# Kernel optimization log

Hardware: AMD Instinct MI355X
Metric: run time of the kernel (lower is better)

The kernel has to match this reference:

```python
import jax, jax.numpy as jnp
import numpy as np

B, T, HS, H, R = 4, 2048, 1024, 16, 16
D = HS // H  # 64 head_dim
LOGIT_01 = float(np.log(0.1 / 0.9))    # g_proj bias init
LOGIT_098 = float(np.log(0.98 / 0.02)) # base decay logits init


def _rope_cos_sin(seq_len, dim, base=10000.0):
    half = dim // 2
    inv_freq = 1.0 / (base ** (jnp.arange(half, dtype=jnp.float32) / half))
    freqs = jnp.arange(seq_len, dtype=jnp.float32)[:, None] * inv_freq[None, :]  # [T, half]
    return jnp.cos(freqs), jnp.sin(freqs)


def _apply_rope(x, cos, sin):
    # x: [B,T,H,D] with D even; rotate interleaved pairs over full D
    c = cos[None, :, None, :]
    s = sin[None, :, None, :]
    x1 = x[..., 0::2]
    x2 = x[..., 1::2]
    r1 = x1 * c - x2 * s
    r2 = x1 * s + x2 * c
    return jnp.stack((r1, r2), axis=-1).reshape(x.shape)


def setup_inputs() -> dict:
    key = jax.random.key(0)
    ks = jax.random.split(key, 10)
    def rn(k, shape, s=0.02):
        return jax.random.normal(k, shape, dtype=jnp.float32) * s
    return {
        "x": jax.random.normal(ks[0], (B, T, HS), dtype=jnp.float32),
        "q_w": rn(ks[1], (HS, HS)),
        "k_w": rn(ks[2], (HS, HS)),
        "v_w": rn(ks[3], (HS, HS)),
        "Wq": rn(ks[4], (H, R, D), 0.05),
        "Wk": rn(ks[5], (H, R, D), 0.05),
        "g_w": rn(ks[6], (H * R, HS)),
        "g_b": jnp.full((H * R,), LOGIT_01, dtype=jnp.float32),
        "base_decay_logits": jnp.full((H, R), LOGIT_098, dtype=jnp.float32),
        "out_w": rn(ks[7], (HS, HS)),
        "out_b": jnp.zeros((HS,), dtype=jnp.float32),
        "ln_g": jnp.ones((HS,), dtype=jnp.float32),
        "ln_b": jnp.zeros((HS,), dtype=jnp.float32),
    }


def reference(x, q_w, k_w, v_w, Wq, Wk, g_w, g_b, base_decay_logits,
              out_w, out_b, ln_g, ln_b):
    b, t, hs = x.shape
    h, r, d = Wq.shape
    # qkv projections (torch Linear: x @ W.T)
    q = (x @ q_w.T).reshape(b, t, h, d)
    k = (x @ k_w.T).reshape(b, t, h, d)
    v = (x @ v_w.T).reshape(b, t, h, d)
    # RoPE (dim_rot == head_dim since it is even)
    cos, sin = _rope_cos_sin(t, d)
    q = _apply_rope(q, cos, sin)
    k = _apply_rope(k, cos, sin)
    # low-rank projections
    q_r = jnp.einsum('bthd,hrd->bthr', q, Wq)
    k_r = jnp.einsum('bthd,hrd->bthr', k, Wk)
    # content gates
    g = jax.nn.sigmoid((x @ g_w.T + g_b).reshape(b, t, h, r))
    decay = jax.nn.sigmoid(base_decay_logits)[None, :, :, None]  # [1,H,r,1]
    scale = 1.0 / jnp.sqrt(jnp.asarray(d, dtype=x.dtype))

    def step(M, inp):
        q_t, k_t, v_t, g_t = inp  # [B,H,r], [B,H,r], [B,H,D], [B,H,r]
        M = M * decay + jnp.einsum('bhr,bhd->bhrd', g_t * k_t * scale, v_t)
        y = jnp.einsum('bhr,bhrd->bhd', q_t, M)
        return M, y

    xs = (q_r.transpose(1, 0, 2, 3), k_r.transpose(1, 0, 2, 3),
          v.transpose(1, 0, 2, 3), g.transpose(1, 0, 2, 3))
    M0 = jnp.zeros((b, h, r, d), dtype=x.dtype)
    _, Y = jax.lax.scan(step, M0, xs)  # Y: [T,B,H,D]
    Y = Y.transpose(1, 0, 2, 3).reshape(b, t, hs)
    out = Y @ out_w.T + out_b  # dropout is identity at eval time
    hres = x + out
    mu = jnp.mean(hres, axis=-1, keepdims=True)
    var = jnp.mean((hres - mu) ** 2, axis=-1, keepdims=True)
    return (hres - mu) / jnp.sqrt(var + 1e-5) * ln_g + ln_b
```

## Files before the change

kernel.cpp:

```cpp
#include <hip/hip_runtime.h>
#include <hip/hip_bf16.h>

#define B_ 4
#define T_ 2048
#define HS_ 1024
#define H_ 16
#define R_ 16
#define D_ 64
#define BT_ (B_*T_)
#define NC_ 3328
#define CHUNK_ 64
#define NCHUNK_ (T_/CHUNK_)

typedef __attribute__((ext_vector_type(8))) short short8;
typedef __attribute__((ext_vector_type(4))) float f32x4;

__device__ __forceinline__ float b2f(ushort u){
    union{unsigned int i; float f;} v; v.i = ((unsigned int)u) << 16; return v.f;
}
__device__ __forceinline__ ushort f2b(float f){
    __hip_bfloat16 h = __float2bfloat16(f);
    return *reinterpret_cast<ushort*>(&h);
}
__device__ __forceinline__ float sigm(float x){ return 1.f/(1.f+expf(-x)); }

__device__ __forceinline__ void gl_lds16(const void* g, void* l){
    __builtin_amdgcn_global_load_lds((const __attribute__((address_space(1))) void*)g,
                                     (__attribute__((address_space(3))) void*)l,
                                     16, 0, 0);
}

__global__ void k_cast4(const float* __restrict__ src, ushort* __restrict__ dst){
    int i = blockIdx.x*256 + threadIdx.x;
    float4 v = ((const float4*)src)[i];
    ushort4 o; o.x=f2b(v.x); o.y=f2b(v.y); o.z=f2b(v.z); o.w=f2b(v.w);
    ((ushort4*)dst)[i] = o;
}

__global__ void k_build_wcat(const float* __restrict__ qw, const float* __restrict__ kw,
                             const float* __restrict__ vw, const float* __restrict__ gw,
                             ushort* __restrict__ wcat){
    int i = blockIdx.x*256 + threadIdx.x;
    int e = i*4;
    int row = e >> 10, col = e & 1023;
    const float* src;
    if      (row < 1024) src = qw + (size_t)row*1024 + col;
    else if (row < 2048) src = kw + (size_t)(row-1024)*1024 + col;
    else if (row < 3072) src = vw + (size_t)(row-2048)*1024 + col;
    else                 src = gw + (size_t)(row-3072)*1024 + col;
    float4 v = *(const float4*)src;
    ushort4 o; o.x=f2b(v.x); o.y=f2b(v.y); o.z=f2b(v.z); o.w=f2b(v.w);
    ((ushort4*)wcat)[i] = o;
}

__global__ void k_rope_tab(float* __restrict__ cosT, float* __restrict__ sinT){
    int i = blockIdx.x*256 + threadIdx.x;
    int t = i >> 5, f = i & 31;
    float inv = powf(10000.f, -(float)f/32.f);
    float a = (float)t * inv;
    cosT[i] = cosf(a);
    sinT[i] = sinf(a);
}

__global__ __launch_bounds__(512, 4) void k_gemm256d(const ushort* __restrict__ A,
                                                     const ushort* __restrict__ Bm,
                                                     ushort* __restrict__ C,
                                                     int K, int ldc){
    __shared__ __align__(16) ushort lds[24576];
    const int tid  = threadIdx.x;
    const int lane = tid & 63, w = tid >> 6;
    const int fr = lane & 15, fg = lane >> 4;
    const int wm = w >> 1, wn = w & 1;
    const int qa = ((fg + fr) & 3) * 8;

    int mt = gridDim.x;
    int L = blockIdx.y * mt + blockIdx.x;
    int bxi, byi;
    int msub = mt >> 3;
    if((mt & 7) == 0 && msub > 0){
        int xcd = L & 7, c = L >> 3;
        bxi = xcd * msub + (c % msub);
        byi = c / msub;
    } else { bxi = blockIdx.x; byi = blockIdx.y; }
    const long arow0 = (long)bxi * 256;
    const long brow0 = (long)byi * 128;

    const int srow = tid >> 2;
    const int scol = ((((tid & 3) - (tid >> 2)) & 3)) * 8;
    const ushort* gsrc0 = A  + (arow0 +       srow) * (size_t)K + scol;
    const ushort* gsrc1 = A  + (arow0 + 128 + srow) * (size_t)K + scol;
    const ushort* gsrc2 = Bm + (brow0 +       srow) * (size_t)K + scol;

#define STG(t) do{ ushort* _b = &lds[((t)&1)*12288 + w*512];                  \
    gl_lds16(gsrc0 + (size_t)(t)*32, _b);                                     \
    gl_lds16(gsrc1 + (size_t)(t)*32, _b + 4096);                              \
    gl_lds16(gsrc2 + (size_t)(t)*32, _b + 8192); }while(0)

    f32x4 acc[4][4];
#pragma unroll
    for(int m=0;m<4;m++)
#pragma unroll
        for(int n=0;n<4;n++)
            acc[m][n] = (f32x4){0.f,0.f,0.f,0.f};

    const int NT = K >> 5;
    STG(0);
    for(int t=0; t<NT; ++t){
        asm volatile("s_waitcnt vmcnt(0)" ::: "memory");
        __builtin_amdgcn_s_barrier();
        __builtin_amdgcn_sched_barrier(0);
        if(t+1 < NT) STG(t+1);
        const int sb = (t&1)*12288;
        short8 af[4], bv[4];
#pragma unroll
        for(int mm=0; mm<4; ++mm)
            af[mm] = *(const short8*)&lds[sb + (wm*64 + mm*16 + fr)*32 + qa];
#pragma unroll
        for(int nf=0; nf<4; ++nf)
            bv[nf] = *(const short8*)&lds[sb + 8192 + (wn*64 + nf*16 + fr)*32 + qa];
        __builtin_amdgcn_s_setprio(1);
#pragma unroll
        for(int mm=0; mm<4; ++mm)
#pragma unroll
        for(int nf=0; nf<4; ++nf)
            acc[mm][nf] = __builtin_amdgcn_mfma_f32_16x16x32_bf16(
                af[mm], bv[nf], acc[mm][nf], 0,0,0);
        __builtin_amdgcn_s_setprio(0);
    }
#undef STG

#pragma unroll
    for(int m=0;m<4;m++)
#pragma unroll
        for(int n=0;n<4;n++){
            long col = brow0 + wn*64 + n*16 + fr;
#pragma unroll
            for(int j=0;j<4;j++){
                long row = arow0 + wm*64 + m*16 + fg*4 + j;
                C[row*(size_t)ldc + col] = f2b(acc[m][n][j]);
            }
        }
}

__global__ __launch_bounds__(256) void k_rope_proj(const ushort* __restrict__ qkvg,
                                                   const float* __restrict__ cosT,
                                                   const float* __restrict__ sinT,
                                                   const float* __restrict__ Wq,
                                                   const float* __restrict__ Wk,
                                                   const float* __restrict__ gb,
                                                   float* __restrict__ qr_s,
                                                   float* __restrict__ gk_s){
    __shared__ __align__(16) ushort lq[64*72], lk[64*72];
    __shared__ __align__(16) ushort wql[16*72], wkl[16*72];
    int tid = threadIdx.x, wid = tid >> 6, lane = tid & 63;
    int bt0 = blockIdx.x * 64;
    int h   = blockIdx.y;

    {
        int row = tid >> 4, seg = tid & 15;
        float4 wq4 = *(const float4*)(Wq + (size_t)h*1024 + row*64 + seg*4);
        float4 wk4 = *(const float4*)(Wk + (size_t)h*1024 + row*64 + seg*4);
        ushort* dq = &wql[row*72 + seg*4];
        ushort* dk = &wkl[row*72 + seg*4];
        dq[0]=f2b(wq4.x); dq[1]=f2b(wq4.y); dq[2]=f2b(wq4.z); dq[3]=f2b(wq4.w);
        dk[0]=f2b(wk4.x); dk[1]=f2b(wk4.y); dk[2]=f2b(wk4.z); dk[3]=f2b(wk4.w);
    }

#pragma unroll
    for(int rep=0; rep<2; ++rep){
        int flat = rep*256 + tid;
        int row = flat >> 3, seg = flat & 7;
        int t = (bt0 + row) & 2047;
        const ushort* base = qkvg + (size_t)(bt0+row)*NC_ + h*64 + seg*8;
        short8 q8 = *(const short8*)base;
        short8 k8 = *(const short8*)(base + 1024);
        float4 cv = *(const float4*)&cosT[t*32 + seg*4];
        float4 sv = *(const float4*)&sinT[t*32 + seg*4];
        float qf[8], kf[8];
#pragma unroll
        for(int j=0;j<8;j++){ qf[j]=b2f((ushort)q8[j]); kf[j]=b2f((ushort)k8[j]); }
        float c4[4] = {cv.x,cv.y,cv.z,cv.w};
        float s4[4] = {sv.x,sv.y,sv.z,sv.w};
        short8 qo, ko;
#pragma unroll
        for(int p=0;p<4;p++){
            float c=c4[p], s=s4[p];
            qo[2*p]   = (short)f2b(qf[2*p]*c - qf[2*p+1]*s);
            qo[2*p+1] = (short)f2b(qf[2*p]*s + qf[2*p+1]*c);
            ko[2*p]   = (short)f2b(kf[2*p]*c - kf[2*p+1]*s);
            ko[2*p+1] = (short)f2b(kf[2*p]*s + kf[2*p+1]*c);
        }
        *(short8*)&lq[row*72 + seg*8] = qo;
        *(short8*)&lk[row*72 + seg*8] = ko;
    }
    __syncthreads();

    int fr = lane & 15, fg = lane >> 4;
    int wrow = wid*16;
    short8 aq0 = *(const short8*)&lq[(wrow+fr)*72 + fg*8];
    short8 aq1 = *(const short8*)&lq[(wrow+fr)*72 + 32 + fg*8];
    short8 ak0 = *(const short8*)&lk[(wrow+fr)*72 + fg*8];
    short8 ak1 = *(const short8*)&lk[(wrow+fr)*72 + 32 + fg*8];
    short8 bq0 = *(const short8*)&wql[fr*72 + fg*8];
    short8 bq1 = *(const short8*)&wql[fr*72 + 32 + fg*8];
    short8 bk0 = *(const short8*)&wkl[fr*72 + fg*8];
    short8 bk1 = *(const short8*)&wkl[fr*72 + 32 + fg*8];
    f32x4 accq = (f32x4){0.f,0.f,0.f,0.f};
    f32x4 acck = (f32x4){0.f,0.f,0.f,0.f};
    accq = __builtin_amdgcn_mfma_f32_16x16x32_bf16(aq0, bq0, accq, 0,0,0);
    accq = __builtin_amdgcn_mfma_f32_16x16x32_bf16(aq1, bq1, accq, 0,0,0);
    acck = __builtin_amdgcn_mfma_f32_16x16x32_bf16(ak0, bk0, acck, 0,0,0);
    acck = __builtin_amdgcn_mfma_f32_16x16x32_bf16(ak1, bk1, acck, 0,0,0);

    int r = fr;
    float gbv = gb[h*16 + r];
#pragma unroll
    for(int j=0;j<4;j++){
        int bt = bt0 + wrow + fg*4 + j;
        int t  = bt & 2047, b = bt >> 11;
        size_t o = (((size_t)(b*16 + h))*2048 + t)*16 + r;
        qr_s[o] = accq[j];
        float gl = b2f(qkvg[(size_t)bt*NC_ + 3072 + h*16 + r]) + gbv;
        gk_s[o] = sigm(gl) * acck[j] * 0.125f;
    }
}

__global__ __launch_bounds__(64) void k_scan_local(const ushort* __restrict__ qkvg,
                                                   const float* __restrict__ gk_s,
                                                   const float* __restrict__ bdl,
                                                   float* __restrict__ Mloc){
    int lane = threadIdx.x;
    int bx = blockIdx.x;
    int ch = bx & (NCHUNK_-1), bh = bx >> 5;
    int b = bh >> 4, h = bh & 15;
    float dec[16], M[16];
#pragma unroll
    for(int r=0;r<16;r++){ dec[r] = sigm(bdl[h*16+r]); M[r] = 0.f; }

    int t0 = ch*CHUNK_;
    const float4*  gk4 = (const float4*)(gk_s + (((size_t)bh)*2048 + t0)*16);
    const ushort*  vp  = qkvg + ((size_t)(b*2048 + t0))*NC_ + 2048 + h*64 + lane;
    for(int tt=0; tt<CHUNK_; ++tt){
        float v = b2f(*vp); vp += NC_;
        float4 a0 = gk4[0], a1 = gk4[1], a2 = gk4[2], a3 = gk4[3]; gk4 += 4;
        float gk[16] = {a0.x,a0.y,a0.z,a0.w, a1.x,a1.y,a1.z,a1.w,
                        a2.x,a2.y,a2.z,a2.w, a3.x,a3.y,a3.z,a3.w};
#pragma unroll
        for(int r=0;r<16;r++) M[r] = fmaf(M[r], dec[r], gk[r]*v);
    }
    float* mp = Mloc + ((size_t)bx)*1024 + lane;
#pragma unroll
    for(int r=0;r<16;r++) mp[r*64] = M[r];
}

__global__ __launch_bounds__(64) void k_scan_carry(float* __restrict__ Mloc,
                                                   const float* __restrict__ bdl){
    int lane = threadIdx.x;
    int sub = blockIdx.x & 3, bh = blockIdx.x >> 2, h = bh & 15;
    float decC[4], S[4];
#pragma unroll
    for(int rr=0;rr<4;rr++){
        decC[rr] = powf(sigm(bdl[h*16 + sub*4 + rr]), (float)CHUNK_);
        S[rr] = 0.f;
    }
    for(int c=0;c<NCHUNK_;c++){
        float* p = Mloc + ((size_t)(bh*NCHUNK_ + c))*1024 + lane + sub*4*64;
#pragma unroll
        for(int rr=0;rr<4;rr++){
            float m = p[rr*64];
            p[rr*64] = S[rr];
            S[rr] = fmaf(S[rr], decC[rr], m);
        }
    }
}

__global__ __launch_bounds__(64) void k_scan_out(const ushort* __restrict__ qkvg,
                                                 const float* __restrict__ gk_s,
                                                 const float* __restrict__ qr_s,
                                                 const float* __restrict__ Mst,
                                                 const float* __restrict__ bdl,
                                                 ushort* __restrict__ Ybf){
    int lane = threadIdx.x;
    int bx = blockIdx.x;
    int ch = bx & (NCHUNK_-1), bh = bx >> 5;
    int b = bh >> 4, h = bh & 15;
    float dec[16], M[16];
#pragma unroll
    for(int r=0;r<16;r++) dec[r] = sigm(bdl[h*16+r]);
    const float* sp = Mst + ((size_t)bx)*1024 + lane;
#pragma unroll
    for(int r=0;r<16;r++) M[r] = sp[r*64];

    int t0 = ch*CHUNK_;
    const float4* gk4 = (const float4*)(gk_s + (((size_t)bh)*2048 + t0)*16);
    const float4* q4  = (const float4*)(qr_s + (((size_t)bh)*2048 + t0)*16);
    const ushort* vp  = qkvg + ((size_t)(b*2048 + t0))*NC_ + 2048 + h*64 + lane;
    ushort*       yp  = Ybf  + ((size_t)(b*2048 + t0))*1024 + h*64 + lane;
    for(int tt=0; tt<CHUNK_; ++tt){
        float v = b2f(*vp); vp += NC_;
        float4 a0 = gk4[0], a1 = gk4[1], a2 = gk4[2], a3 = gk4[3]; gk4 += 4;
        float4 b0 = q4[0],  b1 = q4[1],  b2 = q4[2],  b3 = q4[3];  q4  += 4;
        float gk[16] = {a0.x,a0.y,a0.z,a0.w, a1.x,a1.y,a1.z,a1.w,
                        a2.x,a2.y,a2.z,a2.w, a3.x,a3.y,a3.z,a3.w};
        float qv[16] = {b0.x,b0.y,b0.z,b0.w, b1.x,b1.y,b1.z,b1.w,
                        b2.x,b2.y,b2.z,b2.w, b3.x,b3.y,b3.z,b3.w};
        float y = 0.f;
#pragma unroll
        for(int r=0;r<16;r++){
            M[r] = fmaf(M[r], dec[r], gk[r]*v);
            y    = fmaf(qv[r], M[r], y);
        }
        *yp = f2b(y); yp += 1024;
    }
}

__global__ __launch_bounds__(256) void k_ln(const float* __restrict__ x,
                                            const ushort* __restrict__ O,
                                            const float* __restrict__ ob,
                                            const float* __restrict__ lg,
                                            const float* __restrict__ lb,
                                            float* __restrict__ out){
    __shared__ float red[8];
    int row = blockIdx.x, tid = threadIdx.x;
    float hv[4];
    float sum = 0.f, ssq = 0.f;
#pragma unroll
    for(int k2=0;k2<4;k2++){
        int j = tid + k2*256;
        float v = x[(size_t)row*1024 + j] + b2f(O[(size_t)row*1024 + j]) + ob[j];
        hv[k2] = v; sum += v; ssq += v*v;
    }
#pragma unroll
    for(int off=32; off; off >>= 1){
        sum += __shfl_down(sum, off, 64);
        ssq += __shfl_down(ssq, off, 64);
    }
    int wid = tid >> 6, lane = tid & 63;
    if(lane == 0){ red[wid] = sum; red[4+wid] = ssq; }
    __syncthreads();
    if(tid == 0){
        float s = red[0]+red[1]+red[2]+red[3];
        float q = red[4]+red[5]+red[6]+red[7];
        float mu = s / 1024.f;
        red[0] = mu;
        red[1] = q / 1024.f - mu*mu;
    }
    __syncthreads();
    float mu = red[0];
    float inv = rsqrtf(red[1] + 1e-5f);
#pragma unroll
    for(int k2=0;k2<4;k2++){
        int j = tid + k2*256;
        out[(size_t)row*1024 + j] = (hv[k2]-mu)*inv*lg[j] + lb[j];
    }
}

extern "C" void kernel_launch(void* const* d_in, const int* in_sizes, int n_in,
                              void* d_out, int out_size, void* d_ws, size_t ws_size,
                              hipStream_t stream){
    const float* x    = (const float*)d_in[0];
    const float* q_w  = (const float*)d_in[1];
    const float* k_w  = (const float*)d_in[2];
    const float* v_w  = (const float*)d_in[3];
    const float* Wq   = (const float*)d_in[4];
    const float* Wk   = (const float*)d_in[5];
    const float* g_w  = (const float*)d_in[6];
    const float* g_b  = (const float*)d_in[7];
    const float* bdl  = (const float*)d_in[8];
    const float* outw = (const float*)d_in[9];
    const float* outb = (const float*)d_in[10];
    const float* ln_g = (const float*)d_in[11];
    const float* ln_b = (const float*)d_in[12];
    float* out = (float*)d_out;

    char* ws = (char*)d_ws;
    size_t off = 0;
    ushort* xbf  = (ushort*)(ws + off); off += (size_t)BT_*HS_*2;
    ushort* wcat = (ushort*)(ws + off); off += (size_t)NC_*HS_*2;
    ushort* owbf = (ushort*)(ws + off); off += (size_t)HS_*HS_*2;
    float*  cosT = (float*)(ws + off);  off += (size_t)T_*32*4;
    float*  sinT = (float*)(ws + off);  off += (size_t)T_*32*4;
    ushort* qkvg = (ushort*)(ws + off); off += (size_t)BT_*NC_*2;
    float*  qr_s = (float*)(ws + off);  off += (size_t)BT_*H_*R_*4;
    float*  gk_s = (float*)(ws + off);  off += (size_t)BT_*H_*R_*4;
    float*  Mloc = (float*)(ws + off);  off += (size_t)B_*H_*NCHUNK_*R_*D_*4;
    ushort* Ybf = xbf;
    ushort* O   = qkvg;

    k_cast4<<<(BT_*HS_/4)/256, 256, 0, stream>>>(x, xbf);
    k_build_wcat<<<(NC_*HS_/4)/256, 256, 0, stream>>>(q_w, k_w, v_w, g_w, wcat);
    k_cast4<<<(HS_*HS_/4)/256, 256, 0, stream>>>(outw, owbf);
    k_rope_tab<<<(T_*32)/256, 256, 0, stream>>>(cosT, sinT);

    k_gemm256d<<<dim3(BT_/256, NC_/128), 512, 0, stream>>>(xbf, wcat, qkvg, HS_, NC_);

    k_rope_proj<<<dim3(BT_/64, H_), 256, 0, stream>>>(qkvg, cosT, sinT, Wq, Wk, g_b, qr_s, gk_s);

    k_scan_local<<<B_*H_*NCHUNK_, 64, 0, stream>>>(qkvg, gk_s, bdl, Mloc);
    k_scan_carry<<<B_*H_*4, 64, 0, stream>>>(Mloc, bdl);
    k_scan_out<<<B_*H_*NCHUNK_, 64, 0, stream>>>(qkvg, gk_s, qr_s, Mloc, bdl, Ybf);

    k_gemm256d<<<dim3(BT_/256, HS_/128), 512, 0, stream>>>(Ybf, owbf, O, HS_, HS_);

    k_ln<<<BT_, 256, 0, stream>>>(x, O, outb, ln_g, ln_b, out);

    (void)in_sizes; (void)n_in; (void)out_size; (void)ws_size;
}
```

Measured before the change: 199.7 us.

## Merge prep kernels into one launch and change GEMM LDS swizzle

Combines the four preprocessing kernels (x cast, weight concat cast, out_w cast, RoPE tables) into a single block-ranged kernel so three kernel launches and their gaps disappear. It also changes the LDS swizzle in the GEMM: the store column rotation now uses tid>>3 and the read offset uses fr>>1, which pairs rows for bank-conflict avoidance. The swizzle change must stay consistent between the store and read sides, or results will be wrong.

```diff
diff --git a/kernel.cpp b/kernel.cpp
--- a/kernel.cpp
+++ b/kernel.cpp
@@ -30,36 +30,44 @@
                                      16, 0, 0);
 }
 
-__global__ void k_cast4(const float* __restrict__ src, ushort* __restrict__ dst){
-    int i = blockIdx.x*256 + threadIdx.x;
-    float4 v = ((const float4*)src)[i];
-    ushort4 o; o.x=f2b(v.x); o.y=f2b(v.y); o.z=f2b(v.z); o.w=f2b(v.w);
-    ((ushort4*)dst)[i] = o;
-}
-
-__global__ void k_build_wcat(const float* __restrict__ qw, const float* __restrict__ kw,
-                             const float* __restrict__ vw, const float* __restrict__ gw,
-                             ushort* __restrict__ wcat){
-    int i = blockIdx.x*256 + threadIdx.x;
-    int e = i*4;
-    int row = e >> 10, col = e & 1023;
-    const float* src;
-    if      (row < 1024) src = qw + (size_t)row*1024 + col;
-    else if (row < 2048) src = kw + (size_t)(row-1024)*1024 + col;
-    else if (row < 3072) src = vw + (size_t)(row-2048)*1024 + col;
-    else                 src = gw + (size_t)(row-3072)*1024 + col;
-    float4 v = *(const float4*)src;
-    ushort4 o; o.x=f2b(v.x); o.y=f2b(v.y); o.z=f2b(v.z); o.w=f2b(v.w);
-    ((ushort4*)wcat)[i] = o;
-}
-
-__global__ void k_rope_tab(float* __restrict__ cosT, float* __restrict__ sinT){
-    int i = blockIdx.x*256 + threadIdx.x;
-    int t = i >> 5, f = i & 31;
-    float inv = powf(10000.f, -(float)f/32.f);
-    float a = (float)t * inv;
-    cosT[i] = cosf(a);
-    sinT[i] = sinf(a);
+__global__ void k_prep(const float* __restrict__ x,
+                       const float* __restrict__ qw, const float* __restrict__ kw,
+                       const float* __restrict__ vw, const float* __restrict__ gw,
+                       const float* __restrict__ outw,
+                       ushort* __restrict__ xbf, ushort* __restrict__ wcat,
+                       ushort* __restrict__ owbf,
+                       float* __restrict__ cosT, float* __restrict__ sinT){
+    int bid = blockIdx.x;
+    if(bid < 8192){
+        int i = bid*256 + threadIdx.x;
+        float4 v = ((const float4*)x)[i];
+        ushort4 o; o.x=f2b(v.x); o.y=f2b(v.y); o.z=f2b(v.z); o.w=f2b(v.w);
+        ((ushort4*)xbf)[i] = o;
+    } else if(bid < 11520){
+        int i = (bid-8192)*256 + threadIdx.x;
+        int e = i*4;
+        int row = e >> 10, col = e & 1023;
+        const float* src;
+        if      (row < 1024) src = qw + (size_t)row*1024 + col;
+        else if (row < 2048) src = kw + (size_t)(row-1024)*1024 + col;
+        else if (row < 3072) src = vw + (size_t)(row-2048)*1024 + col;
+        else                 src = gw + (size_t)(row-3072)*1024 + col;
+        float4 v = *(const float4*)src;
+        ushort4 o; o.x=f2b(v.x); o.y=f2b(v.y); o.z=f2b(v.z); o.w=f2b(v.w);
+        ((ushort4*)wcat)[i] = o;
+    } else if(bid < 12544){
+        int i = (bid-11520)*256 + threadIdx.x;
+        float4 v = ((const float4*)outw)[i];
+        ushort4 o; o.x=f2b(v.x); o.y=f2b(v.y); o.z=f2b(v.z); o.w=f2b(v.w);
+        ((ushort4*)owbf)[i] = o;
+    } else {
+        int i = (bid-12544)*256 + threadIdx.x;
+        int t = i >> 5, f = i & 31;
+        float inv = powf(10000.f, -(float)f/32.f);
+        float a = (float)t * inv;
+        cosT[i] = cosf(a);
+        sinT[i] = sinf(a);
+    }
 }
 
 __global__ __launch_bounds__(512, 4) void k_gemm256d(const ushort* __restrict__ A,
@@ -71,7 +79,7 @@
     const int lane = tid & 63, w = tid >> 6;
     const int fr = lane & 15, fg = lane >> 4;
     const int wm = w >> 1, wn = w & 1;
-    const int qa = ((fg + fr) & 3) * 8;
+    const int qa = ((fg + (fr >> 1)) & 3) * 8;
 
     int mt = gridDim.x;
     int L = blockIdx.y * mt + blockIdx.x;
@@ -86,7 +94,7 @@
     const long brow0 = (long)byi * 128;
 
     const int srow = tid >> 2;
-    const int scol = ((((tid & 3) - (tid >> 2)) & 3)) * 8;
+    const int scol = ((((tid & 3) - (tid >> 3)) & 3)) * 8;
     const ushort* gsrc0 = A  + (arow0 +       srow) * (size_t)K + scol;
     const ushort* gsrc1 = A  + (arow0 + 128 + srow) * (size_t)K + scol;
     const ushort* gsrc2 = Bm + (brow0 +       srow) * (size_t)K + scol;
@@ -387,10 +395,8 @@
     ushort* Ybf = xbf;
     ushort* O   = qkvg;
 
-    k_cast4<<<(BT_*HS_/4)/256, 256, 0, stream>>>(x, xbf);
-    k_build_wcat<<<(NC_*HS_/4)/256, 256, 0, stream>>>(q_w, k_w, v_w, g_w, wcat);
-    k_cast4<<<(HS_*HS_/4)/256, 256, 0, stream>>>(outw, owbf);
-    k_rope_tab<<<(T_*32)/256, 256, 0, stream>>>(cosT, sinT);
+    k_prep<<<12800, 256, 0, stream>>>(x, q_w, k_w, v_w, g_w, outw,
+                                      xbf, wcat, owbf, cosT, sinT);
 
     k_gemm256d<<<dim3(BT_/256, NC_/128), 512, 0, stream>>>(xbf, wcat, qkvg, HS_, NC_);
 
```

New measurement: 192.1 us (median of 2 runs). 1.04x faster.
